# Kernel tuning notes

Measured on AMD Instinct MI355X. Metric: run time of the kernel, lower is better.

## Reference

```python
import jax, jax.numpy as jnp
import numpy as np
from jax import lax

INPUT_SIZE = 3
HIDDEN = 32
SEQ = 24
BATCH = 131072
FC1 = 16


def setup_inputs() -> dict:
    key = jax.random.key(0)
    ks = jax.random.split(key, 9)
    s_ih = 1.0 / np.sqrt(HIDDEN)
    # PyTorch LSTM params: weight_ih (4H, input), weight_hh (4H, H), biases (4H,)
    return {
        "x": jax.random.normal(ks[0], (BATCH, SEQ, INPUT_SIZE), dtype=jnp.float32),
        "w_ih": jax.random.uniform(ks[1], (4 * HIDDEN, INPUT_SIZE), minval=-s_ih, maxval=s_ih, dtype=jnp.float32),
        "w_hh": jax.random.uniform(ks[2], (4 * HIDDEN, HIDDEN), minval=-s_ih, maxval=s_ih, dtype=jnp.float32),
        "b_ih": jax.random.uniform(ks[3], (4 * HIDDEN,), minval=-s_ih, maxval=s_ih, dtype=jnp.float32),
        "b_hh": jax.random.uniform(ks[4], (4 * HIDDEN,), minval=-s_ih, maxval=s_ih, dtype=jnp.float32),
        "w1": jax.random.uniform(ks[5], (FC1, HIDDEN), minval=-s_ih, maxval=s_ih, dtype=jnp.float32),
        "b1": jax.random.uniform(ks[6], (FC1,), minval=-s_ih, maxval=s_ih, dtype=jnp.float32),
        "w2": jax.random.uniform(ks[7], (1, FC1), minval=-0.25, maxval=0.25, dtype=jnp.float32),
        "b2": jax.random.uniform(ks[8], (1,), minval=-0.25, maxval=0.25, dtype=jnp.float32),
    }


def reference(x, w_ih, w_hh, b_ih, b_hh, w1, b1, w2, b2):
    B = x.shape[0]
    b = b_ih + b_hh  # fuse the two bias vectors

    def step(carry, xt):
        h, c = carry
        # gates: (B, 4H) in PyTorch order [i, f, g, o]
        gates = xt @ w_ih.T + h @ w_hh.T + b
        i, f, g, o = jnp.split(gates, 4, axis=-1)
        c_new = jax.nn.sigmoid(f) * c + jax.nn.sigmoid(i) * jnp.tanh(g)
        h_new = jax.nn.sigmoid(o) * jnp.tanh(c_new)
        return (h_new, c_new), None

    h0 = jnp.zeros((B, HIDDEN), dtype=x.dtype)
    c0 = jnp.zeros((B, HIDDEN), dtype=x.dtype)
    xs = jnp.transpose(x, (1, 0, 2))  # (T, B, F)
    (h_last, _), _ = lax.scan(step, (h0, c0), xs)

    # Head: Linear(H,16) -> ReLU -> Dropout(identity in eval) -> Linear(16,1)
    hid = jax.nn.relu(h_last @ w1.T + b1)
    logit = hid @ w2.T + b2  # (B, 1)
    return logit
```

## Files before the change

### kernel.cpp

```cpp
#include <hip/hip_runtime.h>


typedef _Float16 f16x8 __attribute__((ext_vector_type(8)));
typedef _Float16 f16x4 __attribute__((ext_vector_type(4)));
typedef _Float16 f16x2 __attribute__((ext_vector_type(2)));
typedef float f32x4 __attribute__((ext_vector_type(4)));
typedef float f32x2 __attribute__((ext_vector_type(2)));

#define L2E 1.4426950408889634f

#if __has_builtin(__builtin_amdgcn_mfma_f32_16x16x16f16)
#define HAVE_MFMA16 1
#else
#define HAVE_MFMA16 0
#endif

__device__ __forceinline__ float fexp2(float v) { return __builtin_amdgcn_exp2f(v); }
__device__ __forceinline__ float frcp(float v)  { return __builtin_amdgcn_rcpf(v); }

__global__ __launch_bounds__(256, 4)
void lstm_fused(const float* __restrict__ x,
                const float* __restrict__ w_ih,
                const float* __restrict__ w_hh,
                const float* __restrict__ b_ih,
                const float* __restrict__ b_hh,
                const float* __restrict__ w1,
                const float* __restrict__ b1,
                const float* __restrict__ w2,
                const float* __restrict__ b2,
                float* __restrict__ out)
{
    __shared__ int2  xq[24 * 64];
    __shared__ float w1s[512];
    __shared__ float b1s[16];
    __shared__ float w2s[16];
    __shared__ float b2s;

    const int tid  = threadIdx.x;
    const int lane = tid & 63;
    const int wv   = tid >> 6;
    const int c    = lane & 15;
    const int g    = lane >> 4;
    const int blockBase = blockIdx.x * 64;

    for (int i = tid; i < 512; i += 256) w1s[i] = w1[i];
    if (tid < 16) { b1s[tid] = b1[tid]; w2s[tid] = w2[tid]; }
    if (tid == 16) b2s = b2[0];

    for (int it = 0; it < 6; ++it) {
        int p = tid + it * 256;
        int n = p / 24;
        int t = p - n * 24;
        const float* xp = x + ((blockBase + n) * 24 + t) * 3;
        union { f16x4 h; int2 i2; } tq;
        tq.h[0] = (_Float16)xp[0];
        tq.h[1] = (_Float16)xp[1];
        tq.h[2] = (_Float16)xp[2];
        tq.h[3] = (_Float16)1.0f;
        xq[t * 64 + n] = tq.i2;
    }

    f16x8 whh[8];
#if HAVE_MFMA16
    f16x4 wib[8];
#else
    f16x8 wib[8];
#endif
    const int ubase = 8 * (c >> 2) + (c & 3);
#pragma unroll
    for (int G = 0; G < 4; ++G) {
        const float scale = (G == 2) ? (2.f * L2E) : L2E;
#pragma unroll
        for (int p = 0; p < 2; ++p) {
            const int row = G * 32 + ubase + 4 * p;
            const float* wr = w_hh + row * 32 + g * 8;
            f16x8 a;
#pragma unroll
            for (int e = 0; e < 8; ++e) a[e] = (_Float16)(wr[e] * scale);
            whh[G * 2 + p] = a;
            _Float16 c0 = 0, c1 = 0, c2 = 0, c3 = 0;
            if (g == 0) {
                c0 = (_Float16)(w_ih[row * 3 + 0] * scale);
                c1 = (_Float16)(w_ih[row * 3 + 1] * scale);
                c2 = (_Float16)(w_ih[row * 3 + 2] * scale);
                c3 = (_Float16)((b_ih[row] + b_hh[row]) * scale);
            }
#if HAVE_MFMA16
            f16x4 bb = {c0, c1, c2, c3};
#else
            f16x8 bb = {c0, c1, c2, c3, 0, 0, 0, 0};
#endif
            wib[G * 2 + p] = bb;
        }
    }

    __syncthreads();

    f32x2 cz = {0.f, 0.f};
    f32x2 cst2[4] = {cz, cz, cz, cz};
    union hu_t { f16x2 p2[4]; f16x8 v; int4 i4; } hreg;
    hreg.i4 = make_int4(0, 0, 0, 0);

    const int n0 = wv * 16 + c;
    int2 xv = xq[n0];

#pragma unroll 1
    for (int t = 0; t < 24; ++t) {
        const int tn = (t < 23) ? t + 1 : 23;
        int2 xnxt = xq[tn * 64 + n0];

        f32x4 acc[2][4];
        const f32x4 z = {0.f, 0.f, 0.f, 0.f};
        f16x8 hf = hreg.v;
#pragma unroll
        for (int p = 0; p < 2; ++p)
#pragma unroll
            for (int G = 0; G < 4; ++G)
                acc[p][G] = __builtin_amdgcn_mfma_f32_16x16x32_f16(
                    whh[2 * G + p], hf, z, 0, 0, 0);
        {
            int xlo = (g == 0) ? xv.x : 0;
            int xhi = (g == 0) ? xv.y : 0;
#if HAVE_MFMA16
            union { int2 i2; f16x4 v; } xu;
            xu.i2 = make_int2(xlo, xhi);
            f16x4 xf = xu.v;
#else
            union { int4 i4; f16x8 v; } xu;
            xu.i4 = make_int4(xlo, xhi, 0, 0);
            f16x8 xf = xu.v;
#endif
#pragma unroll
            for (int p = 0; p < 2; ++p)
#pragma unroll
                for (int G = 0; G < 4; ++G)
#if HAVE_MFMA16
                    acc[p][G] = __builtin_amdgcn_mfma_f32_16x16x16f16(
                        wib[2 * G + p], xf, acc[p][G], 0, 0, 0);
#else
                    acc[p][G] = __builtin_amdgcn_mfma_f32_16x16x32_f16(
                        wib[2 * G + p], xf, acc[p][G], 0, 0, 0);
#endif
        }

        f32x2 ew[4];
#pragma unroll
        for (int q = 0; q < 4; ++q) {
            const int p = q >> 1, j = q & 1;
            ew[q][0] = fexp2(-acc[p][3][2 * j]);
            ew[q][1] = fexp2(-acc[p][3][2 * j + 1]);
        }
        f32x2 ex[4], ey[4], ef[4];
#pragma unroll
        for (int q = 0; q < 4; ++q) {
            const int p = q >> 1, j = q & 1;
            ex[q][0] = fexp2(-acc[p][0][2 * j]); ex[q][1] = fexp2(-acc[p][0][2 * j + 1]);
            ey[q][0] = fexp2( acc[p][2][2 * j]); ey[q][1] = fexp2( acc[p][2][2 * j + 1]);
            ef[q][0] = fexp2(-acc[p][1][2 * j]); ef[q][1] = fexp2(-acc[p][1][2 * j + 1]);
        }
        const f32x2 one = {1.f, 1.f};
        const f32x2 K2  = {2.f * L2E, 2.f * L2E};
        f32x2 axy[4], efp[4], r1[4];
#pragma unroll
        for (int q = 0; q < 4; ++q) {
            axy[q] = (one + ex[q]) * (one + ey[q]);
            efp[q] = one + ef[q];
            f32x2 dd = axy[q] * efp[q];
            r1[q][0] = frcp(dd[0]); r1[q][1] = frcp(dd[1]);
        }
        f32x2 ez[4];
#pragma unroll
        for (int q = 0; q < 4; ++q) {
            f32x2 igs = (ey[q] * K2 - K2) * efp[q] * r1[q];
            f32x2 fs  = axy[q] * r1[q];
            cst2[q] = fs * cst2[q] + igs;
            ez[q][0] = fexp2(cst2[q][0]); ez[q][1] = fexp2(cst2[q][1]);
        }
#pragma unroll
        for (int q = 0; q < 4; ++q) {
            f32x2 d2 = (one + ew[q]) * (one + ez[q]);
            f32x2 r2; r2[0] = frcp(d2[0]); r2[1] = frcp(d2[1]);
            f32x2 hn = (ez[q] - one) * r2;
            f16x2 hh; hh[0] = (_Float16)hn[0]; hh[1] = (_Float16)hn[1];
            hreg.p2[q] = hh;
        }
        xv = xnxt;
    }

    float hfin[8];
#pragma unroll
    for (int d = 0; d < 8; ++d) hfin[d] = (float)hreg.v[d];
    float hid[16];
#pragma unroll
    for (int q = 0; q < 16; ++q) {
        const float4* wrow = (const float4*)(w1s + q * 32 + g * 8);
        float4 wa = wrow[0], wb = wrow[1];
        float sm = wa.x * hfin[0] + wa.y * hfin[1] + wa.z * hfin[2] + wa.w * hfin[3]
                 + wb.x * hfin[4] + wb.y * hfin[5] + wb.z * hfin[6] + wb.w * hfin[7];
        sm += __shfl_xor(sm, 16);
        sm += __shfl_xor(sm, 32);
        hid[q] = sm;
    }
    float po = b2s;
#pragma unroll
    for (int q = 0; q < 16; ++q)
        po = fmaf(fmaxf(hid[q] + b1s[q], 0.f), w2s[q], po);
    if (g == 0) out[blockBase + n0] = po;
}

extern "C" void kernel_launch(void* const* d_in, const int* in_sizes, int n_in,
                              void* d_out, int out_size, void* d_ws, size_t ws_size,
                              hipStream_t stream) {
    (void)in_sizes; (void)n_in; (void)d_ws; (void)ws_size; (void)out_size;
    const float* x    = (const float*)d_in[0];
    const float* w_ih = (const float*)d_in[1];
    const float* w_hh = (const float*)d_in[2];
    const float* b_ih = (const float*)d_in[3];
    const float* b_hh = (const float*)d_in[4];
    const float* w1   = (const float*)d_in[5];
    const float* b1   = (const float*)d_in[6];
    const float* w2   = (const float*)d_in[7];
    const float* b2   = (const float*)d_in[8];
    float* outp = (float*)d_out;

    dim3 grid(131072 / 64);
    dim3 block(256);
    hipLaunchKernelGGL(lstm_fused, grid, block, 0, stream,
                       x, w_ih, w_hh, b_ih, b_hh, w1, b1, w2, b2, outp);
}
```

Measured before the change: 97.42 us.

## Process two independent 16-sample LSTM streams per wave to interleave MFMA and transcendental chains

Each wave now carries two independent sets of 16 batch samples through the recurrence, so each block handles 128 samples and the grid is halved. The two chains are independent, which gives the scheduler room to overlap one stream's MFMA latency with the other's exp/rcp gate math. The cost is higher register pressure (doubled cell and hidden state), which may hurt occupancy under the 256x4 launch bounds. Shared memory for staged inputs doubles as well.

```diff
diff --git a/kernel.cpp b/kernel.cpp
--- a/kernel.cpp
+++ b/kernel.cpp
@@ -30,7 +30,7 @@
                 const float* __restrict__ b2,
                 float* __restrict__ out)
 {
-    __shared__ int2  xq[24 * 64];
+    __shared__ int2  xq[24 * 128];
     __shared__ float w1s[512];
     __shared__ float b1s[16];
     __shared__ float w2s[16];
@@ -41,13 +41,13 @@
     const int wv   = tid >> 6;
     const int c    = lane & 15;
     const int g    = lane >> 4;
-    const int blockBase = blockIdx.x * 64;
+    const int blockBase = blockIdx.x * 128;
 
     for (int i = tid; i < 512; i += 256) w1s[i] = w1[i];
     if (tid < 16) { b1s[tid] = b1[tid]; w2s[tid] = w2[tid]; }
     if (tid == 16) b2s = b2[0];
 
-    for (int it = 0; it < 6; ++it) {
+    for (int it = 0; it < 12; ++it) {
         int p = tid + it * 256;
         int n = p / 24;
         int t = p - n * 24;
@@ -57,7 +57,7 @@
         tq.h[1] = (_Float16)xp[1];
         tq.h[2] = (_Float16)xp[2];
         tq.h[3] = (_Float16)1.0f;
-        xq[t * 64 + n] = tq.i2;
+        xq[t * 128 + n] = tq.i2;
     }
 
     f16x8 whh[8];
@@ -97,115 +97,129 @@
     __syncthreads();
 
     f32x2 cz = {0.f, 0.f};
-    f32x2 cst2[4] = {cz, cz, cz, cz};
-    union hu_t { f16x2 p2[4]; f16x8 v; int4 i4; } hreg;
-    hreg.i4 = make_int4(0, 0, 0, 0);
+    f32x2 cst2[8];
+#pragma unroll
+    for (int q = 0; q < 8; ++q) cst2[q] = cz;
+    union hu_t { f16x2 p2[4]; f16x8 v; int4 i4; } hreg[2];
+    hreg[0].i4 = make_int4(0, 0, 0, 0);
+    hreg[1].i4 = make_int4(0, 0, 0, 0);
 
     const int n0 = wv * 16 + c;
-    int2 xv = xq[n0];
+    int2 xv[2];
+    xv[0] = xq[n0];
+    xv[1] = xq[n0 + 64];
 
 #pragma unroll 1
     for (int t = 0; t < 24; ++t) {
         const int tn = (t < 23) ? t + 1 : 23;
-        int2 xnxt = xq[tn * 64 + n0];
-
-        f32x4 acc[2][4];
-        const f32x4 z = {0.f, 0.f, 0.f, 0.f};
-        f16x8 hf = hreg.v;
-#pragma unroll
-        for (int p = 0; p < 2; ++p)
-#pragma unroll
-            for (int G = 0; G < 4; ++G)
-                acc[p][G] = __builtin_amdgcn_mfma_f32_16x16x32_f16(
-                    whh[2 * G + p], hf, z, 0, 0, 0);
-        {
-            int xlo = (g == 0) ? xv.x : 0;
-            int xhi = (g == 0) ? xv.y : 0;
-#if HAVE_MFMA16
-            union { int2 i2; f16x4 v; } xu;
-            xu.i2 = make_int2(xlo, xhi);
-            f16x4 xf = xu.v;
-#else
-            union { int4 i4; f16x8 v; } xu;
-            xu.i4 = make_int4(xlo, xhi, 0, 0);
-            f16x8 xf = xu.v;
-#endif
+        int2 xn0 = xq[tn * 128 + n0];
+        int2 xn1 = xq[tn * 128 + n0 + 64];
+
+#pragma unroll
+        for (int s = 0; s < 2; ++s) {
+            f32x4 acc[2][4];
+            const f32x4 z = {0.f, 0.f, 0.f, 0.f};
+            f16x8 hf = hreg[s].v;
 #pragma unroll
             for (int p = 0; p < 2; ++p)
 #pragma unroll
                 for (int G = 0; G < 4; ++G)
-#if HAVE_MFMA16
-                    acc[p][G] = __builtin_amdgcn_mfma_f32_16x16x16f16(
-                        wib[2 * G + p], xf, acc[p][G], 0, 0, 0);
-#else
                     acc[p][G] = __builtin_amdgcn_mfma_f32_16x16x32_f16(
-                        wib[2 * G + p], xf, acc[p][G], 0, 0, 0);
-#endif
+                        whh[2 * G + p], hf, z, 0, 0, 0);
+            {
+                int xlo = (g == 0) ? xv[s].x : 0;
+                int xhi = (g == 0) ? xv[s].y : 0;
+#if HAVE_MFMA16
+                union { int2 i2; f16x4 v; } xu;
+                xu.i2 = make_int2(xlo, xhi);
+                f16x4 xf = xu.v;
+#else
+                union { int4 i4; f16x8 v; } xu;
+                xu.i4 = make_int4(xlo, xhi, 0, 0);
+                f16x8 xf = xu.v;
+#endif
+#pragma unroll
+                for (int p = 0; p < 2; ++p)
+#pragma unroll
+                    for (int G = 0; G < 4; ++G)
+#if HAVE_MFMA16
+                        acc[p][G] = __builtin_amdgcn_mfma_f32_16x16x16f16(
+                            wib[2 * G + p], xf, acc[p][G], 0, 0, 0);
+#else
+                        acc[p][G] = __builtin_amdgcn_mfma_f32_16x16x32_f16(
+                            wib[2 * G + p], xf, acc[p][G], 0, 0, 0);
+#endif
+            }
+
+            f32x2 ew[4];
+#pragma unroll
+            for (int q = 0; q < 4; ++q) {
+                const int p = q >> 1, j = q & 1;
+                ew[q][0] = fexp2(-acc[p][3][2 * j]);
+                ew[q][1] = fexp2(-acc[p][3][2 * j + 1]);
+            }
+            f32x2 ex[4], ey[4], ef[4];
+#pragma unroll
+            for (int q = 0; q < 4; ++q) {
+                const int p = q >> 1, j = q & 1;
+                ex[q][0] = fexp2(-acc[p][0][2 * j]); ex[q][1] = fexp2(-acc[p][0][2 * j + 1]);
+                ey[q][0] = fexp2( acc[p][2][2 * j]); ey[q][1] = fexp2( acc[p][2][2 * j + 1]);
+                ef[q][0] = fexp2(-acc[p][1][2 * j]); ef[q][1] = fexp2(-acc[p][1][2 * j + 1]);
+            }
+            const f32x2 one = {1.f, 1.f};
+            const f32x2 K2  = {2.f * L2E, 2.f * L2E};
+            f32x2 axy[4], efp[4], r1[4];
+#pragma unroll
+            for (int q = 0; q < 4; ++q) {
+                axy[q] = (one + ex[q]) * (one + ey[q]);
+                efp[q] = one + ef[q];
+                f32x2 dd = axy[q] * efp[q];
+                r1[q][0] = frcp(dd[0]); r1[q][1] = frcp(dd[1]);
+            }
+            f32x2 ez[4];
+#pragma unroll
+            for (int q = 0; q < 4; ++q) {
+                f32x2 igs = (ey[q] * K2 - K2) * efp[q] * r1[q];
+                f32x2 fs  = axy[q] * r1[q];
+                cst2[s * 4 + q] = fs * cst2[s * 4 + q] + igs;
+                ez[q][0] = fexp2(cst2[s * 4 + q][0]);
+                ez[q][1] = fexp2(cst2[s * 4 + q][1]);
+            }
+#pragma unroll
+            for (int q = 0; q < 4; ++q) {
+                f32x2 d2 = (one + ew[q]) * (one + ez[q]);
+                f32x2 r2; r2[0] = frcp(d2[0]); r2[1] = frcp(d2[1]);
+                f32x2 hn = (ez[q] - one) * r2;
+                f16x2 hh; hh[0] = (_Float16)hn[0]; hh[1] = (_Float16)hn[1];
+                hreg[s].p2[q] = hh;
+            }
         }
-
-        f32x2 ew[4];
-#pragma unroll
-        for (int q = 0; q < 4; ++q) {
-            const int p = q >> 1, j = q & 1;
-            ew[q][0] = fexp2(-acc[p][3][2 * j]);
-            ew[q][1] = fexp2(-acc[p][3][2 * j + 1]);
+        xv[0] = xn0;
+        xv[1] = xn1;
+    }
+
+#pragma unroll
+    for (int s = 0; s < 2; ++s) {
+        float hfin[8];
+#pragma unroll
+        for (int d = 0; d < 8; ++d) hfin[d] = (float)hreg[s].v[d];
+        float hid[16];
+#pragma unroll
+        for (int q = 0; q < 16; ++q) {
+            const float4* wrow = (const float4*)(w1s + q * 32 + g * 8);
+            float4 wa = wrow[0], wb = wrow[1];
+            float sm = wa.x * hfin[0] + wa.y * hfin[1] + wa.z * hfin[2] + wa.w * hfin[3]
+                     + wb.x * hfin[4] + wb.y * hfin[5] + wb.z * hfin[6] + wb.w * hfin[7];
+            sm += __shfl_xor(sm, 16);
+            sm += __shfl_xor(sm, 32);
+            hid[q] = sm;
         }
-        f32x2 ex[4], ey[4], ef[4];
-#pragma unroll
-        for (int q = 0; q < 4; ++q) {
-            const int p = q >> 1, j = q & 1;
-            ex[q][0] = fexp2(-acc[p][0][2 * j]); ex[q][1] = fexp2(-acc[p][0][2 * j + 1]);
-            ey[q][0] = fexp2( acc[p][2][2 * j]); ey[q][1] = fexp2( acc[p][2][2 * j + 1]);
-            ef[q][0] = fexp2(-acc[p][1][2 * j]); ef[q][1] = fexp2(-acc[p][1][2 * j + 1]);
-        }
-        const f32x2 one = {1.f, 1.f};
-        const f32x2 K2  = {2.f * L2E, 2.f * L2E};
-        f32x2 axy[4], efp[4], r1[4];
-#pragma unroll
-        for (int q = 0; q < 4; ++q) {
-            axy[q] = (one + ex[q]) * (one + ey[q]);
-            efp[q] = one + ef[q];
-            f32x2 dd = axy[q] * efp[q];
-            r1[q][0] = frcp(dd[0]); r1[q][1] = frcp(dd[1]);
-        }
-        f32x2 ez[4];
-#pragma unroll
-        for (int q = 0; q < 4; ++q) {
-            f32x2 igs = (ey[q] * K2 - K2) * efp[q] * r1[q];
-            f32x2 fs  = axy[q] * r1[q];
-            cst2[q] = fs * cst2[q] + igs;
-            ez[q][0] = fexp2(cst2[q][0]); ez[q][1] = fexp2(cst2[q][1]);
-        }
-#pragma unroll
-        for (int q = 0; q < 4; ++q) {
-            f32x2 d2 = (one + ew[q]) * (one + ez[q]);
-            f32x2 r2; r2[0] = frcp(d2[0]); r2[1] = frcp(d2[1]);
-            f32x2 hn = (ez[q] - one) * r2;
-            f16x2 hh; hh[0] = (_Float16)hn[0]; hh[1] = (_Float16)hn[1];
-            hreg.p2[q] = hh;
-        }
-        xv = xnxt;
-    }
-
-    float hfin[8];
-#pragma unroll
-    for (int d = 0; d < 8; ++d) hfin[d] = (float)hreg.v[d];
-    float hid[16];
-#pragma unroll
-    for (int q = 0; q < 16; ++q) {
-        const float4* wrow = (const float4*)(w1s + q * 32 + g * 8);
-        float4 wa = wrow[0], wb = wrow[1];
-        float sm = wa.x * hfin[0] + wa.y * hfin[1] + wa.z * hfin[2] + wa.w * hfin[3]
-                 + wb.x * hfin[4] + wb.y * hfin[5] + wb.z * hfin[6] + wb.w * hfin[7];
-        sm += __shfl_xor(sm, 16);
-        sm += __shfl_xor(sm, 32);
-        hid[q] = sm;
-    }
-    float po = b2s;
-#pragma unroll
-    for (int q = 0; q < 16; ++q)
-        po = fmaf(fmaxf(hid[q] + b1s[q], 0.f), w2s[q], po);
-    if (g == 0) out[blockBase + n0] = po;
+        float po = b2s;
+#pragma unroll
+        for (int q = 0; q < 16; ++q)
+            po = fmaf(fmaxf(hid[q] + b1s[q], 0.f), w2s[q], po);
+        if (g == 0) out[blockBase + s * 64 + n0] = po;
+    }
 }
 
 extern "C" void kernel_launch(void* const* d_in, const int* in_sizes, int n_in,
@@ -223,7 +237,7 @@
     const float* b2   = (const float*)d_in[8];
     float* outp = (float*)d_out;
 
-    dim3 grid(131072 / 64);
+    dim3 grid(131072 / 128);
     dim3 block(256);
     hipLaunchKernelGGL(lstm_fused, grid, block, 0, stream,
                        x, w_ih, w_hh, b_ih, b_hh, w1, b1, w2, b2, outp);
```

Result: slower. 101.1 us (+3.7%).

## Move W_hh fragments to shared memory to raise occupancy

Applied to the files above, without the earlier changes.

Recurrent weight fragments, previously held in registers per thread, now live in LDS: the first wave converts them once and every step reloads them with ds_read before the MFMAs. This frees about 32 VGPRs so launch bounds can rise to 5 blocks per CU. The head weights are read straight from global memory instead of being staged in LDS, which keeps the LDS footprint down. In exchange each timestep adds LDS reads on the serial recurrence path.

```diff
diff --git a/kernel.cpp b/kernel.cpp
--- a/kernel.cpp
+++ b/kernel.cpp
@@ -18,7 +18,7 @@
 __device__ __forceinline__ float fexp2(float v) { return __builtin_amdgcn_exp2f(v); }
 __device__ __forceinline__ float frcp(float v)  { return __builtin_amdgcn_rcpf(v); }
 
-__global__ __launch_bounds__(256, 4)
+__global__ __launch_bounds__(256, 5)
 void lstm_fused(const float* __restrict__ x,
                 const float* __restrict__ w_ih,
                 const float* __restrict__ w_hh,
@@ -30,11 +30,8 @@
                 const float* __restrict__ b2,
                 float* __restrict__ out)
 {
-    __shared__ int2  xq[24 * 64];
-    __shared__ float w1s[512];
-    __shared__ float b1s[16];
-    __shared__ float w2s[16];
-    __shared__ float b2s;
+    __shared__ int2 xq[24 * 64];
+    __shared__ int4 whhs[8 * 64];
 
     const int tid  = threadIdx.x;
     const int lane = tid & 63;
@@ -42,10 +39,6 @@
     const int c    = lane & 15;
     const int g    = lane >> 4;
     const int blockBase = blockIdx.x * 64;
-
-    for (int i = tid; i < 512; i += 256) w1s[i] = w1[i];
-    if (tid < 16) { b1s[tid] = b1[tid]; w2s[tid] = w2[tid]; }
-    if (tid == 16) b2s = b2[0];
 
     for (int it = 0; it < 6; ++it) {
         int p = tid + it * 256;
@@ -60,24 +53,34 @@
         xq[t * 64 + n] = tq.i2;
     }
 
-    f16x8 whh[8];
+    const int ubase = 8 * (c >> 2) + (c & 3);
+    if (tid < 64) {
+#pragma unroll
+        for (int G = 0; G < 4; ++G) {
+            const float scale = (G == 2) ? (2.f * L2E) : L2E;
+#pragma unroll
+            for (int p = 0; p < 2; ++p) {
+                const int row = G * 32 + ubase + 4 * p;
+                const float* wr = w_hh + row * 32 + g * 8;
+                union { f16x8 h; int4 i4; } a;
+#pragma unroll
+                for (int e = 0; e < 8; ++e) a.h[e] = (_Float16)(wr[e] * scale);
+                whhs[(G * 2 + p) * 64 + c * 4 + g] = a.i4;
+            }
+        }
+    }
+
 #if HAVE_MFMA16
     f16x4 wib[8];
 #else
     f16x8 wib[8];
 #endif
-    const int ubase = 8 * (c >> 2) + (c & 3);
 #pragma unroll
     for (int G = 0; G < 4; ++G) {
         const float scale = (G == 2) ? (2.f * L2E) : L2E;
 #pragma unroll
         for (int p = 0; p < 2; ++p) {
             const int row = G * 32 + ubase + 4 * p;
-            const float* wr = w_hh + row * 32 + g * 8;
-            f16x8 a;
-#pragma unroll
-            for (int e = 0; e < 8; ++e) a[e] = (_Float16)(wr[e] * scale);
-            whh[G * 2 + p] = a;
             _Float16 c0 = 0, c1 = 0, c2 = 0, c3 = 0;
             if (g == 0) {
                 c0 = (_Float16)(w_ih[row * 3 + 0] * scale);
@@ -103,21 +106,27 @@
 
     const int n0 = wv * 16 + c;
     int2 xv = xq[n0];
+    unsigned woff = (unsigned)(c * 4 + g);
 
 #pragma unroll 1
     for (int t = 0; t < 24; ++t) {
         const int tn = (t < 23) ? t + 1 : 23;
         int2 xnxt = xq[tn * 64 + n0];
 
+        asm volatile("" : "+v"(woff));
+
         f32x4 acc[2][4];
         const f32x4 z = {0.f, 0.f, 0.f, 0.f};
         f16x8 hf = hreg.v;
 #pragma unroll
         for (int p = 0; p < 2; ++p)
 #pragma unroll
-            for (int G = 0; G < 4; ++G)
+            for (int G = 0; G < 4; ++G) {
+                union { int4 i4; f16x8 h; } fr;
+                fr.i4 = whhs[(2 * G + p) * 64 + woff];
                 acc[p][G] = __builtin_amdgcn_mfma_f32_16x16x32_f16(
-                    whh[2 * G + p], hf, z, 0, 0, 0);
+                    fr.h, hf, z, 0, 0, 0);
+            }
         {
             int xlo = (g == 0) ? xv.x : 0;
             int xhi = (g == 0) ? xv.y : 0;
@@ -193,7 +202,7 @@
     float hid[16];
 #pragma unroll
     for (int q = 0; q < 16; ++q) {
-        const float4* wrow = (const float4*)(w1s + q * 32 + g * 8);
+        const float4* wrow = (const float4*)(w1 + q * 32 + g * 8);
         float4 wa = wrow[0], wb = wrow[1];
         float sm = wa.x * hfin[0] + wa.y * hfin[1] + wa.z * hfin[2] + wa.w * hfin[3]
                  + wb.x * hfin[4] + wb.y * hfin[5] + wb.z * hfin[6] + wb.w * hfin[7];
@@ -201,10 +210,10 @@
         sm += __shfl_xor(sm, 32);
         hid[q] = sm;
     }
-    float po = b2s;
+    float po = b2[0];
 #pragma unroll
     for (int q = 0; q < 16; ++q)
-        po = fmaf(fmaxf(hid[q] + b1s[q], 0.f), w2s[q], po);
+        po = fmaf(fmaxf(hid[q] + b1[q], 0.f), w2[q], po);
     if (g == 0) out[blockBase + n0] = po;
 }
 
```

Result: faster. 94.55 us (-2.9%).
